# Kernel tuning notes

Measured on AMD Instinct MI355X. Metric: run time of the kernel, lower is better.

Reference implementation:

```python
import jax, jax.numpy as jnp
import numpy as np

FACTOR = 2  # upsample factor per spatial dim


def setup_inputs() -> dict:
    key = jax.random.key(0)
    k1, k2, k3 = jax.random.split(key, 3)
    B, C_in, C_out, H, W_ = 8, 128, 128, 64, 64
    x = jax.random.normal(k1, (B, C_in, H, W_), dtype=jnp.float32)
    # conv3x3 params (OIHW), fan-in scaled init like torch Conv2d default scale
    fan_in = C_in * 3 * 3
    W = jax.random.normal(k2, (C_out, C_in, 3, 3), dtype=jnp.float32) / np.sqrt(fan_in)
    b = jax.random.normal(k3, (C_out,), dtype=jnp.float32) * 0.01
    return {"x": x, "W": W, "b": b}


def reference(x, W, b):
    h = jnp.repeat(jnp.repeat(x, FACTOR, axis=2), FACTOR, axis=3)  # [B,C,2H,2W]
    # conv3x3: stride 1, padding 1
    out = jax.lax.conv_general_dilated(
        h, W,
        window_strides=(1, 1),
        padding=((1, 1), (1, 1)),
        dimension_numbers=("NCHW", "OIHW", "NCHW"),
    )
    return out + b[None, :, None, None]
```

## Files before the change

### kernel.cpp

```cpp
#include <hip/hip_runtime.h>
#include <stdint.h>

typedef short bf16x8 __attribute__((ext_vector_type(8)));
typedef float f32x4 __attribute__((ext_vector_type(4)));
typedef unsigned int u32x4 __attribute__((ext_vector_type(4)));

#define NCI 128
#define NCO 128
#define HIN 64
#define HP  66
#define NB  8

__device__ __forceinline__ unsigned short f32_to_bf16(float f) {
    union { float f; uint32_t u; } v; v.f = f;
    return (unsigned short)((v.u + 0x7FFFu + ((v.u >> 16) & 1u)) >> 16);
}

__device__ __forceinline__ void gl_lds16(const void* g, void* l) {
    __builtin_amdgcn_global_load_lds(
        (const __attribute__((address_space(1))) unsigned int*)g,
        (__attribute__((address_space(3))) unsigned int*)l, 16, 0, 0);
}

__device__ __forceinline__ void vmw0() {
    asm volatile("s_waitcnt vmcnt(0)" ::: "memory");
}
__device__ __forceinline__ void lkw0() {
    asm volatile("s_waitcnt lgkmcnt(0)" ::: "memory");
}
__device__ __forceinline__ void barx() {
    asm volatile("" ::: "memory");
    __builtin_amdgcn_s_barrier();
    asm volatile("" ::: "memory");
}

__global__ __launch_bounds__(256) void prep_kernel(
        const float* __restrict__ W, const float* __restrict__ x,
        unsigned short* __restrict__ Aw2, unsigned short* __restrict__ xq) {
    if (blockIdx.x < 1024) {
        int idx = blockIdx.x * 256 + threadIdx.x;
        int e   = idx & 7;
        int pp  = (idx >> 3) & 3;
        int row = (idx >> 5) & 127;
        int kt  = (idx >> 12) & 15;
        int par = idx >> 16;
        int k   = kt * 32 + ((pp ^ ((row >> 1) & 3)) * 8) + e;
        int tap = k >> 7, ci = k & 127;
        int ty = tap >> 1, tx = tap & 1;
        int py = par >> 1, px = par & 1;
        const float* wp = W + (row * NCI + ci) * 9;
        float s = 0.f;
        #pragma unroll
        for (int ky = 0; ky < 3; ++ky) {
            bool iy = (py == 0) ? (ty == 0 ? (ky == 0) : (ky >= 1))
                                : (ty == 0 ? (ky <= 1) : (ky == 2));
            if (!iy) continue;
            #pragma unroll
            for (int kx = 0; kx < 3; ++kx) {
                bool ix = (px == 0) ? (tx == 0 ? (kx == 0) : (kx >= 1))
                                    : (tx == 0 ? (kx <= 1) : (kx == 2));
                if (ix) s += wp[ky * 3 + kx];
            }
        }
        Aw2[idx] = f32_to_bf16(s);
    } else {
        const int bb = blockIdx.x - 1024;
        const int b = bb / HP, hp = bb % HP;
        const int t = threadIdx.x;
        if (hp == 0 || hp == HP - 1) {
            bf16x8 z = (bf16x8){0, 0, 0, 0, 0, 0, 0, 0};
            for (int i = t; i < 4 * HP * 4; i += 256) {
                int g = i / (HP * 4), rem = i % (HP * 4);
                unsigned short* dst = xq +
                    ((((size_t)(b * 4 + g) * HP + hp) * HP) << 5) + rem * 8;
                *(bf16x8*)dst = z;
            }
            return;
        }
        const int h = hp - 1;
        if (t < 32) {
            bf16x8 z = (bf16x8){0, 0, 0, 0, 0, 0, 0, 0};
            int g = t >> 3, wpc = ((t >> 2) & 1) * (HP - 1), q = t & 3;
            unsigned short* dst = xq +
                ((((size_t)(b * 4 + g) * HP + hp) * HP + wpc) << 5) + q * 8;
            *(bf16x8*)dst = z;
        }
        const int w = t & 63, g = t >> 6;
        const float* src = x + ((size_t)(b * NCI + g * 32) * (HIN * HIN)) + h * HIN + w;
        unsigned short* dst = xq +
            ((((size_t)(b * 4 + g) * HP + hp) * HP + (w + 1)) << 5);
        #pragma unroll
        for (int q = 0; q < 4; ++q) {
            bf16x8 v;
            #pragma unroll
            for (int j = 0; j < 8; ++j)
                v[j] = (short)f32_to_bf16(src[(size_t)(q * 8 + j) * (HIN * HIN)]);
            *(bf16x8*)(dst + q * 8) = v;
        }
    }
}

__global__ __launch_bounds__(512, 2) void upconv4_kernel(
        const unsigned short* __restrict__ xq, const unsigned short* __restrict__ Aw2,
        const float* __restrict__ bv, float* __restrict__ out) {
    __shared__ __align__(16) unsigned short smem[32768];
    unsigned short* sA = smem;
    unsigned short* sB = smem + 16384;
    const int d = blockIdx.x;
    const int ds = (d & 7) * 64 + (d >> 3);
    const int tile = ds >> 1, py = ds & 1;
    const int bi = tile >> 5;
    const int oy0 = (tile & 31) * 2;
    const int tid = threadIdx.x, lane = tid & 63, wv = tid >> 6;
    const int pxw = wv >> 2, wm = (wv >> 1) & 1, wn = wv & 1;

    const int srow = tid >> 2;
    const int pL = (tid & 3) ^ ((srow >> 1) & 3);
    const int box = srow & 63;
    const int boy = oy0 + (srow >> 6);

    f32x4 acc[4][4];
    #pragma unroll
    for (int i = 0; i < 4; ++i)
        #pragma unroll
        for (int j = 0; j < 4; ++j)
            acc[i][j] = (f32x4){0.f, 0.f, 0.f, 0.f};

    auto stage = [&](int buf, int kt2) {
        const int g = kt2 & 3, tx = (kt2 >> 2) & 1, ty = kt2 >> 3;
        const int rowg = boy + py + ty;
        #pragma unroll
        for (int px = 0; px < 2; ++px) {
            const unsigned short* ga =
                Aw2 + ((((py * 2 + px) * 16 + kt2) << 12)) + tid * 8;
            gl_lds16(ga, &sA[(buf * 2 + px) * 4096 + tid * 8]);
            const int wpn = box + px + tx;
            const unsigned short* gb = xq +
                ((((size_t)(bi * 4 + g) * HP + rowg) * HP + wpn) << 5) + pL * 8;
            gl_lds16(gb, &sB[(buf * 2 + px) * 4096 + tid * 8]);
        }
    };

    const int rl = lane & 15, pl = lane >> 4;

    stage(0, 0);
    vmw0();
    barx();

    int cur = 0;
    for (int kt = 0; kt < 16; ++kt) {
        if (kt < 15) stage(cur ^ 1, kt + 1);
        bf16x8 af[4], bfr[4];
        #pragma unroll
        for (int f = 0; f < 4; ++f) {
            int ar = wm * 64 + f * 16 + rl;
            af[f] = *(const bf16x8*)&sA[(cur * 2 + pxw) * 4096 + ar * 32 +
                                        ((pl ^ ((ar >> 1) & 3)) * 8)];
            int bn = wn * 64 + f * 16 + rl;
            bfr[f] = *(const bf16x8*)&sB[(cur * 2 + pxw) * 4096 + bn * 32 +
                                         ((pl ^ ((bn >> 1) & 3)) * 8)];
        }
        #pragma unroll
        for (int fm = 0; fm < 4; ++fm)
            #pragma unroll
            for (int fn = 0; fn < 4; ++fn)
                acc[fm][fn] = __builtin_amdgcn_mfma_f32_16x16x32_bf16(
                    af[fm], bfr[fn], acc[fm][fn], 0, 0, 0);
        vmw0();
        barx();
        cur ^= 1;
    }

    float* lf = (float*)smem;
    const int co_l = tid >> 4;
    const int rem = tid & 15, rr = rem >> 3, x16 = (rem & 7) * 16;
    const int co_g = (co_l >> 4) * 64 + (co_l & 15);
    const int yy = 2 * (oy0 + rr) + py;

    #pragma unroll
    for (int fm = 0; fm < 4; ++fm) {
        #pragma unroll
        for (int fn = 0; fn < 4; ++fn) {
            int n = wn * 64 + fn * 16 + rl;
            int r = n >> 6, xx = 2 * (n & 63) + pxw;
            #pragma unroll
            for (int j = 0; j < 4; ++j) {
                int col = wm * 16 + pl * 4 + j;
                lf[col * 264 + r * 132 + xx] = acc[fm][fn][j];
            }
        }
        lkw0();
        barx();
        const int co = co_g + fm * 16;
        const float bb = bv[co];
        float* op = out + (((size_t)bi * NCO + co) * 128 + yy) * 128 + x16;
        const float* sp = lf + co_l * 264 + rr * 132 + x16;
        #pragma unroll
        for (int q = 0; q < 4; ++q) {
            f32x4 v = *(const f32x4*)(sp + q * 4);
            v[0] += bb; v[1] += bb; v[2] += bb; v[3] += bb;
            *(f32x4*)(op + q * 4) = v;
        }
        if (fm < 3) barx();
    }
}

__global__ __launch_bounds__(256) void upconv_fb_kernel(
        const float* __restrict__ x, const unsigned short* __restrict__ Aw2,
        const float* __restrict__ bv, float* __restrict__ out) {
    __shared__ __align__(16) unsigned short A_lds[128 * 32];
    __shared__ __align__(16) unsigned short B_lds[128 * 32];
    const int par = blockIdx.y, py = par >> 1, px = par & 1;
    const int s0 = blockIdx.x * 128;
    const int bimg = s0 >> 12;
    const int oy0 = (s0 >> 6) & 63;
    const int tid = threadIdx.x;
    const int lane = tid & 63, wave = tid >> 6;
    const int wm = wave >> 1, wn = wave & 1;
    const float* xb = x + bimg * (NCI * HIN * HIN);
    f32x4 acc[4][4];
    #pragma unroll
    for (int i = 0; i < 4; ++i)
        #pragma unroll
        for (int j = 0; j < 4; ++j)
            acc[i][j] = (f32x4){0.f, 0.f, 0.f, 0.f};
    for (int kt = 0; kt < 16; ++kt) {
        const int tap = kt >> 2, ci0 = (kt & 3) * 32;
        const int ty = tap >> 1, tx = tap & 1;
        #pragma unroll
        for (int i = 0; i < 2; ++i) {
            int c = i * 256 + tid;
            *(bf16x8*)(&A_lds[c * 8]) =
                *(const bf16x8*)(Aw2 + ((par * 16 + kt) << 12) + c * 8);
        }
        #pragma unroll
        for (int i = 0; i < 2; ++i) {
            int tsk = i * 256 + tid;
            int n = tsk & 127, kg = tsk >> 7;
            int r = n >> 6, ox = n & 63;
            int row = oy0 + r - 1 + py + ty;
            int col = ox - 1 + px + tx;
            bool ok = (row >= 0) & (row < HIN) & (col >= 0) & (col < HIN);
            const float* xp = xb + (((ci0 + kg * 8) * HIN + row) * HIN + col);
            bf16x8 v;
            #pragma unroll
            for (int q = 0; q < 8; ++q) {
                float f = ok ? xp[q * (HIN * HIN)] : 0.f;
                v[q] = (short)f32_to_bf16(f);
            }
            *(bf16x8*)(&B_lds[n * 32 + kg * 8]) = v;
        }
        __syncthreads();
        const int rl2 = lane & 15, pl2 = lane >> 4;
        bf16x8 af[4], bfr[4];
        #pragma unroll
        for (int f = 0; f < 4; ++f) {
            int ar = wm * 64 + f * 16 + rl2;
            af[f] = *(const bf16x8*)(&A_lds[ar * 32 + ((pl2 ^ ((ar >> 1) & 3)) * 8)]);
            bfr[f] = *(const bf16x8*)(&B_lds[(wn * 64 + f * 16 + rl2) * 32 + pl2 * 8]);
        }
        #pragma unroll
        for (int fm = 0; fm < 4; ++fm)
            #pragma unroll
            for (int fn = 0; fn < 4; ++fn)
                acc[fm][fn] = __builtin_amdgcn_mfma_f32_16x16x32_bf16(
                    af[fm], bfr[fn], acc[fm][fn], 0, 0, 0);
        __syncthreads();
    }
    #pragma unroll
    for (int fm = 0; fm < 4; ++fm) {
        const int co_b = wm * 64 + fm * 16 + (lane >> 4) * 4;
        float bias4[4];
        #pragma unroll
        for (int j = 0; j < 4; ++j) bias4[j] = bv[co_b + j];
        #pragma unroll
        for (int fn = 0; fn < 4; ++fn) {
            int n = wn * 64 + fn * 16 + (lane & 15);
            int s = s0 + n;
            int ox = s & 63, oy = (s >> 6) & 63, bi2 = s >> 12;
            int yy = 2 * oy + py, xx = 2 * ox + px;
            float* op = out + ((size_t)bi2 * 128 * 128 * 128) + (size_t)yy * 128 + xx;
            #pragma unroll
            for (int j = 0; j < 4; ++j)
                op[(size_t)(co_b + j) * (128 * 128)] = acc[fm][fn][j] + bias4[j];
        }
    }
}

extern "C" void kernel_launch(void* const* d_in, const int* in_sizes, int n_in,
                              void* d_out, int out_size, void* d_ws, size_t ws_size,
                              hipStream_t stream) {
    const float* x  = (const float*)d_in[0];
    const float* W  = (const float*)d_in[1];
    const float* bv = (const float*)d_in[2];
    float* out = (float*)d_out;
    unsigned short* Aw2 = (unsigned short*)d_ws;
    const size_t aw_bytes = 4 * 16 * 128 * 32 * sizeof(unsigned short);
    const size_t xq_bytes = (size_t)NB * 4 * HP * HP * 32 * sizeof(unsigned short);

    if (ws_size >= aw_bytes + xq_bytes) {
        unsigned short* xq = (unsigned short*)((char*)d_ws + aw_bytes);
        prep_kernel<<<1024 + NB * HP, 256, 0, stream>>>(W, x, Aw2, xq);
        upconv4_kernel<<<512, 512, 0, stream>>>(xq, Aw2, bv, out);
    } else {
        prep_kernel<<<1024, 256, 0, stream>>>(W, x, Aw2, (unsigned short*)nullptr);
        upconv_fb_kernel<<<dim3(256, 4), 256, 0, stream>>>(x, Aw2, bv, out);
    }
}
```

Baseline: 49.11 us.

## Load weights straight to registers and triple-buffer input tiles in LDS

Weight fragments are now read directly from global memory into double-buffered registers instead of being staged through LDS. Only the input tiles are staged in LDS, using a three-stage ring with partial vmcnt waits so loads for two steps ahead overlap the MFMAs. The launch bound also asks for four blocks per CU, which caps per-thread registers while the 64-float accumulator array plus prefetched fragments need many, so spills are a risk. With only 512 blocks in the grid, the extra occupancy may not be usable anyway.

```diff
diff --git a/kernel.cpp b/kernel.cpp
--- a/kernel.cpp
+++ b/kernel.cpp
@@ -22,9 +22,6 @@
         (__attribute__((address_space(3))) unsigned int*)l, 16, 0, 0);
 }
 
-__device__ __forceinline__ void vmw0() {
-    asm volatile("s_waitcnt vmcnt(0)" ::: "memory");
-}
 __device__ __forceinline__ void lkw0() {
     asm volatile("s_waitcnt lgkmcnt(0)" ::: "memory");
 }
@@ -100,25 +97,26 @@
     }
 }
 
-__global__ __launch_bounds__(512, 2) void upconv4_kernel(
+__global__ __launch_bounds__(512, 4) void upconv5_kernel(
         const unsigned short* __restrict__ xq, const unsigned short* __restrict__ Aw2,
         const float* __restrict__ bv, float* __restrict__ out) {
-    __shared__ __align__(16) unsigned short smem[32768];
-    unsigned short* sA = smem;
-    unsigned short* sB = smem + 16384;
+    __shared__ __align__(16) unsigned short smem[3 * 2 * 4096];
     const int d = blockIdx.x;
-    const int ds = (d & 7) * 64 + (d >> 3);
-    const int tile = ds >> 1, py = ds & 1;
+    const int dsw = (d & 7) * 64 + (d >> 3);
+    const int tile = dsw >> 1, py = dsw & 1;
     const int bi = tile >> 5;
     const int oy0 = (tile & 31) * 2;
     const int tid = threadIdx.x, lane = tid & 63, wv = tid >> 6;
     const int pxw = wv >> 2, wm = (wv >> 1) & 1, wn = wv & 1;
+    const int rl = lane & 15, pl = lane >> 4;
 
     const int srow = tid >> 2;
     const int pL = (tid & 3) ^ ((srow >> 1) & 3);
     const int box = srow & 63;
     const int boy = oy0 + (srow >> 6);
 
+    const unsigned short* Abase = Aw2 + (((py * 2 + pxw) * 16) << 12);
+
     f32x4 acc[4][4];
     #pragma unroll
     for (int i = 0; i < 4; ++i)
@@ -126,49 +124,55 @@
         for (int j = 0; j < 4; ++j)
             acc[i][j] = (f32x4){0.f, 0.f, 0.f, 0.f};
 
-    auto stage = [&](int buf, int kt2) {
-        const int g = kt2 & 3, tx = (kt2 >> 2) & 1, ty = kt2 >> 3;
+    auto stageB = [&](int st, int kt) {
+        const int g = kt & 3, tx = (kt >> 2) & 1, ty = kt >> 3;
         const int rowg = boy + py + ty;
         #pragma unroll
         for (int px = 0; px < 2; ++px) {
-            const unsigned short* ga =
-                Aw2 + ((((py * 2 + px) * 16 + kt2) << 12)) + tid * 8;
-            gl_lds16(ga, &sA[(buf * 2 + px) * 4096 + tid * 8]);
-            const int wpn = box + px + tx;
             const unsigned short* gb = xq +
-                ((((size_t)(bi * 4 + g) * HP + rowg) * HP + wpn) << 5) + pL * 8;
-            gl_lds16(gb, &sB[(buf * 2 + px) * 4096 + tid * 8]);
+                ((((size_t)(bi * 4 + g) * HP + rowg) * HP + (box + px + tx)) << 5) + pL * 8;
+            gl_lds16(gb, &smem[(st * 2 + px) * 4096 + tid * 8]);
         }
     };
-
-    const int rl = lane & 15, pl = lane >> 4;
-
-    stage(0, 0);
-    vmw0();
-    barx();
-
-    int cur = 0;
-    for (int kt = 0; kt < 16; ++kt) {
-        if (kt < 15) stage(cur ^ 1, kt + 1);
-        bf16x8 af[4], bfr[4];
+    auto loadA = [&](bf16x8* Adst, int kt) {
         #pragma unroll
         for (int f = 0; f < 4; ++f) {
             int ar = wm * 64 + f * 16 + rl;
-            af[f] = *(const bf16x8*)&sA[(cur * 2 + pxw) * 4096 + ar * 32 +
-                                        ((pl ^ ((ar >> 1) & 3)) * 8)];
+            Adst[f] = *(const bf16x8*)(Abase + (kt << 12) + ar * 32 +
+                                       ((pl ^ ((ar >> 1) & 3)) * 8));
+        }
+    };
+
+    bf16x8 A0[4], A1[4];
+    stageB(0, 0);
+    stageB(1, 1);
+    loadA(A0, 0);
+    asm volatile("s_waitcnt vmcnt(6)" ::: "memory");
+    barx();
+
+    #pragma unroll
+    for (int t = 0; t < 16; ++t) {
+        if (t + 2 < 16) stageB((t + 2) % 3, t + 2);
+        if (t + 1 < 16) loadA((t & 1) ? A0 : A1, t + 1);
+        if (t <= 13)      { asm volatile("s_waitcnt vmcnt(6)" ::: "memory"); }
+        else if (t == 14) { asm volatile("s_waitcnt vmcnt(4)" ::: "memory"); }
+        else              { asm volatile("s_waitcnt vmcnt(0)" ::: "memory"); }
+
+        const unsigned short* sb = &smem[(((t % 3) * 2 + pxw) * 4096)];
+        bf16x8 bfr[4];
+        #pragma unroll
+        for (int f = 0; f < 4; ++f) {
             int bn = wn * 64 + f * 16 + rl;
-            bfr[f] = *(const bf16x8*)&sB[(cur * 2 + pxw) * 4096 + bn * 32 +
-                                         ((pl ^ ((bn >> 1) & 3)) * 8)];
-        }
+            bfr[f] = *(const bf16x8*)&sb[bn * 32 + ((pl ^ ((bn >> 1) & 3)) * 8)];
+        }
+        const bf16x8* Ac = (t & 1) ? A1 : A0;
         #pragma unroll
         for (int fm = 0; fm < 4; ++fm)
             #pragma unroll
             for (int fn = 0; fn < 4; ++fn)
                 acc[fm][fn] = __builtin_amdgcn_mfma_f32_16x16x32_bf16(
-                    af[fm], bfr[fn], acc[fm][fn], 0, 0, 0);
-        vmw0();
+                    Ac[fm], bfr[fn], acc[fm][fn], 0, 0, 0);
         barx();
-        cur ^= 1;
     }
 
     float* lf = (float*)smem;
@@ -301,7 +305,7 @@
     if (ws_size >= aw_bytes + xq_bytes) {
         unsigned short* xq = (unsigned short*)((char*)d_ws + aw_bytes);
         prep_kernel<<<1024 + NB * HP, 256, 0, stream>>>(W, x, Aw2, xq);
-        upconv4_kernel<<<512, 512, 0, stream>>>(xq, Aw2, bv, out);
+        upconv5_kernel<<<512, 512, 0, stream>>>(xq, Aw2, bv, out);
     } else {
         prep_kernel<<<1024, 256, 0, stream>>>(W, x, Aw2, (unsigned short*)nullptr);
         upconv_fb_kernel<<<dim3(256, 4), 256, 0, stream>>>(x, Aw2, bv, out);
```

New measurement: 119.1 us. 2.42x slower.

## Double K-step depth per stage in upconv kernel with 128KB LDS tiles

Applied to the files above, without the earlier changes.

The main GEMM kernel now stages 64-wide K slices (8 stages instead of 16) with a wider 8-way XOR swizzle, doubling LDS use to 128KB per block and halving the number of barrier/wait points. The weight prep layout is changed to match, and the fallback path gets its own flat weight layout kernel. Fewer synchronisations per tile reduce pipeline stalls, but the larger LDS footprint may lower occupancy below the two blocks per CU requested.

```diff
diff --git a/kernel.cpp b/kernel.cpp
--- a/kernel.cpp
+++ b/kernel.cpp
@@ -3,7 +3,6 @@
 
 typedef short bf16x8 __attribute__((ext_vector_type(8)));
 typedef float f32x4 __attribute__((ext_vector_type(4)));
-typedef unsigned int u32x4 __attribute__((ext_vector_type(4)));
 
 #define NCI 128
 #define NCO 128
@@ -34,35 +33,39 @@
     asm volatile("" ::: "memory");
 }
 
+__device__ __forceinline__ float weff_sum(const float* wp, int py, int px, int ty, int tx) {
+    float s = 0.f;
+    #pragma unroll
+    for (int ky = 0; ky < 3; ++ky) {
+        bool iy = (py == 0) ? (ty == 0 ? (ky == 0) : (ky >= 1))
+                            : (ty == 0 ? (ky <= 1) : (ky == 2));
+        if (!iy) continue;
+        #pragma unroll
+        for (int kx = 0; kx < 3; ++kx) {
+            bool ix = (px == 0) ? (tx == 0 ? (kx == 0) : (kx >= 1))
+                                : (tx == 0 ? (kx <= 1) : (kx == 2));
+            if (ix) s += wp[ky * 3 + kx];
+        }
+    }
+    return s;
+}
+
 __global__ __launch_bounds__(256) void prep_kernel(
         const float* __restrict__ W, const float* __restrict__ x,
-        unsigned short* __restrict__ Aw2, unsigned short* __restrict__ xq) {
+        unsigned short* __restrict__ Aw3, unsigned short* __restrict__ xq) {
     if (blockIdx.x < 1024) {
         int idx = blockIdx.x * 256 + threadIdx.x;
         int e   = idx & 7;
-        int pp  = (idx >> 3) & 3;
-        int row = (idx >> 5) & 127;
-        int kt  = (idx >> 12) & 15;
+        int s   = (idx >> 3) & 1023;
+        int u   = (idx >> 13) & 7;
         int par = idx >> 16;
-        int k   = kt * 32 + ((pp ^ ((row >> 1) & 3)) * 8) + e;
+        int row = s >> 3, partP = s & 7;
+        int partL = partP ^ (row & 7);
+        int k = u * 64 + partL * 8 + e;
         int tap = k >> 7, ci = k & 127;
         int ty = tap >> 1, tx = tap & 1;
         int py = par >> 1, px = par & 1;
-        const float* wp = W + (row * NCI + ci) * 9;
-        float s = 0.f;
-        #pragma unroll
-        for (int ky = 0; ky < 3; ++ky) {
-            bool iy = (py == 0) ? (ty == 0 ? (ky == 0) : (ky >= 1))
-                                : (ty == 0 ? (ky <= 1) : (ky == 2));
-            if (!iy) continue;
-            #pragma unroll
-            for (int kx = 0; kx < 3; ++kx) {
-                bool ix = (px == 0) ? (tx == 0 ? (kx == 0) : (kx >= 1))
-                                    : (tx == 0 ? (kx <= 1) : (kx == 2));
-                if (ix) s += wp[ky * 3 + kx];
-            }
-        }
-        Aw2[idx] = f32_to_bf16(s);
+        Aw3[idx] = f32_to_bf16(weff_sum(W + (row * NCI + ci) * 9, py, px, ty, tx));
     } else {
         const int bb = blockIdx.x - 1024;
         const int b = bb / HP, hp = bb % HP;
@@ -100,24 +103,18 @@
     }
 }
 
-__global__ __launch_bounds__(512, 2) void upconv4_kernel(
-        const unsigned short* __restrict__ xq, const unsigned short* __restrict__ Aw2,
+__global__ __launch_bounds__(512, 2) void upconv8_kernel(
+        const unsigned short* __restrict__ xq, const unsigned short* __restrict__ Aw3,
         const float* __restrict__ bv, float* __restrict__ out) {
-    __shared__ __align__(16) unsigned short smem[32768];
-    unsigned short* sA = smem;
-    unsigned short* sB = smem + 16384;
+    __shared__ __align__(16) unsigned short smem[65536];
     const int d = blockIdx.x;
-    const int ds = (d & 7) * 64 + (d >> 3);
-    const int tile = ds >> 1, py = ds & 1;
+    const int dsw = (d & 7) * 64 + (d >> 3);
+    const int tile = dsw >> 1, py = dsw & 1;
     const int bi = tile >> 5;
     const int oy0 = (tile & 31) * 2;
     const int tid = threadIdx.x, lane = tid & 63, wv = tid >> 6;
     const int pxw = wv >> 2, wm = (wv >> 1) & 1, wn = wv & 1;
-
-    const int srow = tid >> 2;
-    const int pL = (tid & 3) ^ ((srow >> 1) & 3);
-    const int box = srow & 63;
-    const int boy = oy0 + (srow >> 6);
+    const int rl = lane & 15, pl = lane >> 4;
 
     f32x4 acc[4][4];
     #pragma unroll
@@ -126,49 +123,57 @@
         for (int j = 0; j < 4; ++j)
             acc[i][j] = (f32x4){0.f, 0.f, 0.f, 0.f};
 
-    auto stage = [&](int buf, int kt2) {
-        const int g = kt2 & 3, tx = (kt2 >> 2) & 1, ty = kt2 >> 3;
-        const int rowg = boy + py + ty;
+    auto stage = [&](int c, int u) {
+        const int tap = u >> 1, ty = tap >> 1, tx = tap & 1;
+        const int gb0 = (u & 1) * 2;
         #pragma unroll
         for (int px = 0; px < 2; ++px) {
-            const unsigned short* ga =
-                Aw2 + ((((py * 2 + px) * 16 + kt2) << 12)) + tid * 8;
-            gl_lds16(ga, &sA[(buf * 2 + px) * 4096 + tid * 8]);
-            const int wpn = box + px + tx;
-            const unsigned short* gb = xq +
-                ((((size_t)(bi * 4 + g) * HP + rowg) * HP + wpn) << 5) + pL * 8;
-            gl_lds16(gb, &sB[(buf * 2 + px) * 4096 + tid * 8]);
+            const int par = py * 2 + px;
+            #pragma unroll
+            for (int h = 0; h < 2; ++h) {
+                const int s = tid + h * 512;
+                const unsigned short* ga = Aw3 + (((par * 8 + u) << 13) + s * 8);
+                gl_lds16(ga, &smem[(((c * 2 + 0) * 2 + px) << 13) + s * 8]);
+                const int row = s >> 3, partP = s & 7;
+                const int partL = partP ^ (row & 7);
+                const int g = gb0 + (partL >> 2), off = (partL & 3) * 8;
+                const int rowg = oy0 + (row >> 6) + py + ty;
+                const int col = (row & 63) + px + tx;
+                const unsigned short* gb = xq +
+                    ((((size_t)(bi * 4 + g) * HP + rowg) * HP + col) << 5) + off;
+                gl_lds16(gb, &smem[(((c * 2 + 1) * 2 + px) << 13) + s * 8]);
+            }
         }
     };
-
-    const int rl = lane & 15, pl = lane >> 4;
 
     stage(0, 0);
     vmw0();
     barx();
 
-    int cur = 0;
-    for (int kt = 0; kt < 16; ++kt) {
-        if (kt < 15) stage(cur ^ 1, kt + 1);
-        bf16x8 af[4], bfr[4];
-        #pragma unroll
-        for (int f = 0; f < 4; ++f) {
-            int ar = wm * 64 + f * 16 + rl;
-            af[f] = *(const bf16x8*)&sA[(cur * 2 + pxw) * 4096 + ar * 32 +
-                                        ((pl ^ ((ar >> 1) & 3)) * 8)];
-            int bn = wn * 64 + f * 16 + rl;
-            bfr[f] = *(const bf16x8*)&sB[(cur * 2 + pxw) * 4096 + bn * 32 +
-                                         ((pl ^ ((bn >> 1) & 3)) * 8)];
-        }
-        #pragma unroll
-        for (int fm = 0; fm < 4; ++fm)
-            #pragma unroll
-            for (int fn = 0; fn < 4; ++fn)
-                acc[fm][fn] = __builtin_amdgcn_mfma_f32_16x16x32_bf16(
-                    af[fm], bfr[fn], acc[fm][fn], 0, 0, 0);
-        vmw0();
-        barx();
-        cur ^= 1;
+    #pragma unroll 2
+    for (int u = 0; u < 8; ++u) {
+        const int cur = u & 1;
+        if (u < 7) stage(cur ^ 1, u + 1);
+        const unsigned short* sa = &smem[((cur * 2 + 0) * 2 + pxw) << 13];
+        const unsigned short* sb = &smem[((cur * 2 + 1) * 2 + pxw) << 13];
+        #pragma unroll
+        for (int kk = 0; kk < 2; ++kk) {
+            bf16x8 af[4], bfr[4];
+            #pragma unroll
+            for (int f = 0; f < 4; ++f) {
+                int ar = wm * 64 + f * 16 + rl;
+                af[f] = *(const bf16x8*)&sa[ar * 64 + (((kk * 4 + pl) ^ (ar & 7)) * 8)];
+                int bn = wn * 64 + f * 16 + rl;
+                bfr[f] = *(const bf16x8*)&sb[bn * 64 + (((kk * 4 + pl) ^ (bn & 7)) * 8)];
+            }
+            #pragma unroll
+            for (int fm = 0; fm < 4; ++fm)
+                #pragma unroll
+                for (int fn = 0; fn < 4; ++fn)
+                    acc[fm][fn] = __builtin_amdgcn_mfma_f32_16x16x32_bf16(
+                        af[fm], bfr[fn], acc[fm][fn], 0, 0, 0);
+        }
+        if (u < 7) { vmw0(); barx(); }
     }
 
     float* lf = (float*)smem;
@@ -205,8 +210,19 @@
     }
 }
 
+__global__ void weff_flat_kernel(const float* __restrict__ W,
+                                 unsigned short* __restrict__ Aw) {
+    int idx = blockIdx.x * 256 + threadIdx.x;
+    int par = idx >> 16;
+    int co  = (idx >> 9) & 127;
+    int k   = idx & 511;
+    int tap = k >> 7, ci = k & 127;
+    Aw[idx] = f32_to_bf16(weff_sum(W + (co * NCI + ci) * 9,
+                                   par >> 1, par & 1, tap >> 1, tap & 1));
+}
+
 __global__ __launch_bounds__(256) void upconv_fb_kernel(
-        const float* __restrict__ x, const unsigned short* __restrict__ Aw2,
+        const float* __restrict__ x, const unsigned short* __restrict__ Aw,
         const float* __restrict__ bv, float* __restrict__ out) {
     __shared__ __align__(16) unsigned short A_lds[128 * 32];
     __shared__ __align__(16) unsigned short B_lds[128 * 32];
@@ -230,8 +246,8 @@
         #pragma unroll
         for (int i = 0; i < 2; ++i) {
             int c = i * 256 + tid;
-            *(bf16x8*)(&A_lds[c * 8]) =
-                *(const bf16x8*)(Aw2 + ((par * 16 + kt) << 12) + c * 8);
+            *(bf16x8*)(&A_lds[c * 8]) = *(const bf16x8*)(Aw +
+                ((par * 128 + (c >> 2)) * 512 + kt * 32 + (c & 3) * 8));
         }
         #pragma unroll
         for (int i = 0; i < 2; ++i) {
@@ -251,14 +267,14 @@
             *(bf16x8*)(&B_lds[n * 32 + kg * 8]) = v;
         }
         __syncthreads();
-        const int rl2 = lane & 15, pl2 = lane >> 4;
+        const int seg = (lane >> 4) * 8, rl2 = lane & 15;
         bf16x8 af[4], bfr[4];
         #pragma unroll
-        for (int f = 0; f < 4; ++f) {
-            int ar = wm * 64 + f * 16 + rl2;
-            af[f] = *(const bf16x8*)(&A_lds[ar * 32 + ((pl2 ^ ((ar >> 1) & 3)) * 8)]);
-            bfr[f] = *(const bf16x8*)(&B_lds[(wn * 64 + f * 16 + rl2) * 32 + pl2 * 8]);
-        }
+        for (int f = 0; f < 4; ++f)
+            af[f] = *(const bf16x8*)(&A_lds[(wm * 64 + f * 16 + rl2) * 32 + seg]);
+        #pragma unroll
+        for (int f = 0; f < 4; ++f)
+            bfr[f] = *(const bf16x8*)(&B_lds[(wn * 64 + f * 16 + rl2) * 32 + seg]);
         #pragma unroll
         for (int fm = 0; fm < 4; ++fm)
             #pragma unroll
@@ -294,16 +310,16 @@
     const float* W  = (const float*)d_in[1];
     const float* bv = (const float*)d_in[2];
     float* out = (float*)d_out;
-    unsigned short* Aw2 = (unsigned short*)d_ws;
-    const size_t aw_bytes = 4 * 16 * 128 * 32 * sizeof(unsigned short);
+    unsigned short* Aw = (unsigned short*)d_ws;
+    const size_t aw_bytes = (size_t)4 * 8 * 8192 * sizeof(unsigned short);
     const size_t xq_bytes = (size_t)NB * 4 * HP * HP * 32 * sizeof(unsigned short);
 
     if (ws_size >= aw_bytes + xq_bytes) {
         unsigned short* xq = (unsigned short*)((char*)d_ws + aw_bytes);
-        prep_kernel<<<1024 + NB * HP, 256, 0, stream>>>(W, x, Aw2, xq);
-        upconv4_kernel<<<512, 512, 0, stream>>>(xq, Aw2, bv, out);
+        prep_kernel<<<1024 + NB * HP, 256, 0, stream>>>(W, x, Aw, xq);
+        upconv8_kernel<<<512, 512, 0, stream>>>(xq, Aw, bv, out);
     } else {
-        prep_kernel<<<1024, 256, 0, stream>>>(W, x, Aw2, (unsigned short*)nullptr);
-        upconv_fb_kernel<<<dim3(256, 4), 256, 0, stream>>>(x, Aw2, bv, out);
-    }
-}
+        weff_flat_kernel<<<1024, 256, 0, stream>>>(W, Aw);
+        upconv_fb_kernel<<<dim3(256, 4), 256, 0, stream>>>(x, Aw, bv, out);
+    }
+}
```

Result: slower. 54.94 us (+11.9%).
